# Kernel tuning notes

Measured on AMD Instinct MI355X. Metric: run time of the kernel, lower is better.

## Reference

```python
import jax, jax.numpy as jnp
import numpy as np

M0 = 0.5
M_MIN = 0.25
SCALE = 32.0
NUM_CLASSES = 100000
FEAT_DIM = 256
BATCH = 512


def setup_inputs() -> dict:
    key = jax.random.key(0)
    k1, k2, k3, k4 = jax.random.split(key, 4)
    features = jax.random.normal(k1, (BATCH, FEAT_DIM), dtype=jnp.float32)
    labels = jax.random.randint(k2, (BATCH,), 0, NUM_CLASSES, dtype=jnp.int64)
    weights = jax.random.uniform(k3, (BATCH,), dtype=jnp.float32)
    # xavier_uniform for (num_classes, feat_dim)
    limit = float(np.sqrt(6.0 / (NUM_CLASSES + FEAT_DIM)))
    weight = jax.random.uniform(k4, (NUM_CLASSES, FEAT_DIM), dtype=jnp.float32,
                                minval=-limit, maxval=limit)
    return {"features": features, "weight": weight, "weights": weights, "labels": labels}


def reference(features, weight, weights, labels):
    B = features.shape[0]
    norms = jnp.linalg.norm(features, axis=1)  # (B,)
    lo = jax.lax.stop_gradient(norms.min())
    hi = jax.lax.stop_gradient(norms.max())
    denom = jnp.maximum(hi - lo, 1e-8)
    margins = jnp.clip(M_MIN + (M0 - M_MIN) * (norms - lo) / denom, M_MIN, M0)  # (B,)

    feat_n = features / jnp.maximum(norms, 1e-12)[:, None]
    w_n = weight / jnp.maximum(jnp.linalg.norm(weight, axis=1), 1e-12)[:, None]
    cosine = jnp.clip(feat_n @ w_n.T, -1.0 + 1e-7, 1.0 - 1e-7)  # (B, C)

    rows = jnp.arange(B)
    cos_t = cosine[rows, labels]                      # target cosine (B,)
    theta_t = jnp.arccos(cos_t)
    cos_m_t = cos_t * jnp.cos(margins) - jnp.sin(theta_t) * jnp.sin(margins)

    logits = SCALE * cosine
    logits = logits.at[rows, labels].set(SCALE * cos_m_t)

    logp = jax.nn.log_softmax(logits, axis=1)
    per_sample = -logp[rows, labels]
    return (per_sample * weights).mean()
```

## Files before the change

kernel.cpp:

```cpp
#include <hip/hip_runtime.h>
#include <hip/hip_bf16.h>
#include <math.h>

#define BATCH 512
#define FEAT  256
#define NCLS  100000
#define SCALE_ 32.0f
#define M0_    0.5f
#define MMIN_  0.25f

#define BN 32
#define NT32 3125
#define NSLOTS 256
#define NPART 256
#define K4CHUNK 16
#define NK4 (NPART / K4CHUNK)

#define LOG2E_ 1.44269504088896f
#define K2C_   (SCALE_ * LOG2E_)

typedef unsigned short u16;
typedef short s16x8 __attribute__((ext_vector_type(8)));
typedef float f32x4 __attribute__((ext_vector_type(4)));

__device__ u16   g_fbf16[BATCH * FEAT];
__device__ float g_norms[BATCH];
__device__ float g_dot[BATCH];
__device__ float g_wn2[BATCH];
__device__ float g_psum[NPART * BATCH];
__device__ float g_qs[NK4 * BATCH];

__device__ __forceinline__ u16 f2b(float x) {
  union { float f; unsigned u; } v; v.f = x;
  unsigned r = v.u + 0x7FFFu + ((v.u >> 16) & 1u);
  return (u16)(r >> 16);
}

__device__ __forceinline__ unsigned pkbf16(float a, float b) {
  unsigned r;
  asm("v_cvt_pk_bf16_f32 %0, %1, %2" : "=v"(r) : "v"(a), "v"(b));
  return r;
}

__device__ __forceinline__ float ex2(float x) {
  return __builtin_amdgcn_exp2f(x);
}

__global__ void k12(const float* __restrict__ feat, const float* __restrict__ wmat,
                    const void* __restrict__ labels) {
  int b = blockIdx.x;
  int wid = threadIdx.x >> 6, lane = threadIdx.x & 63;
  if (b < 128) {
    int row = b * 4 + wid;
    float4 f = ((const float4*)(feat + row * FEAT))[lane];
    float ss = f.x * f.x + f.y * f.y + f.z * f.z + f.w * f.w;
    #pragma unroll
    for (int d = 1; d < 64; d <<= 1) ss += __shfl_xor(ss, d, 64);
    float nrm = sqrtf(ss);
    float inv = 1.0f / fmaxf(nrm, 1e-12f);
    ushort4 h;
    h.x = f2b(f.x * inv); h.y = f2b(f.y * inv);
    h.z = f2b(f.z * inv); h.w = f2b(f.w * inv);
    ((ushort4*)(g_fbf16 + row * FEAT))[lane] = h;
    if (lane == 0) g_norms[row] = nrm;
  } else {
    int i = (b - 128) * 4 + wid;
    const int* labw = (const int*)labels;
    int odd = 0;
    #pragma unroll
    for (int k = 0; k < 4; ++k) odd |= labw[2 * (k * 64 + lane) + 1];
    unsigned long long bl = __ballot(odd != 0);
    long long lab;
    if (bl != 0ULL) lab = (long long)((const int*)labels)[i];
    else            lab = ((const long long*)labels)[i];
    float4 a = ((const float4*)(feat + i * FEAT))[lane];
    float4 w = ((const float4*)(wmat + (size_t)lab * FEAT))[lane];
    float d  = a.x * w.x + a.y * w.y + a.z * w.z + a.w * w.w;
    float bb = w.x * w.x + w.y * w.y + w.z * w.z + w.w * w.w;
    #pragma unroll
    for (int t = 1; t < 64; t <<= 1) {
      d  += __shfl_xor(d, t, 64);
      bb += __shfl_xor(bb, t, 64);
    }
    if (lane == 0) { g_dot[i] = d; g_wn2[i] = bb; }
  }
}


#define LOADC(TILE) do {                                                    \
    rowL_ = tid >> 4;                                                       \
    const float4* s0_ = (const float4*)(wmat + (size_t)((TILE) * BN + rowL_) * FEAT + (tid & 15) * 16);      \
    const float4* s1_ = (const float4*)(wmat + (size_t)((TILE) * BN + 16 + rowL_) * FEAT + (tid & 15) * 16); \
    v_[0] = s0_[0]; v_[1] = s0_[1]; v_[2] = s0_[2]; v_[3] = s0_[3];         \
    v_[4] = s1_[0]; v_[5] = s1_[1]; v_[6] = s1_[2]; v_[7] = s1_[3];         \
  } while (0)

#define FINHALF(NB, G, ROW) do {                                            \
    float ss_ = 0.0f;                                                       \
    _Pragma("unroll")                                                       \
    for (int k_ = 0; k_ < 4; ++k_) {                                        \
      float4 vv_ = v_[(G) * 4 + k_];                                        \
      ss_ += vv_.x * vv_.x + vv_.y * vv_.y + vv_.z * vv_.z + vv_.w * vv_.w; \
    }                                                                       \
    ss_ += __shfl_xor(ss_, 1, 64);                                          \
    ss_ += __shfl_xor(ss_, 2, 64);                                          \
    ss_ += __shfl_xor(ss_, 4, 64);                                          \
    ss_ += __shfl_xor(ss_, 8, 64);                                          \
    float inv_ = 1.0f / fmaxf(sqrtf(ss_), 1e-12f);                          \
    u16* dst_ = &Ws[NB][0] + (ROW) * FEAT;                                  \
    _Pragma("unroll")                                                       \
    for (int k_ = 0; k_ < 2; ++k_) {                                        \
      int jj_ = (tid & 15) * 2 + k_;                                        \
      float4 va_ = v_[(G) * 4 + 2 * k_], vb_ = v_[(G) * 4 + 2 * k_ + 1];    \
      int4 w4_;                                                             \
      w4_.x = (int)pkbf16(va_.x * inv_, va_.y * inv_);                      \
      w4_.y = (int)pkbf16(va_.z * inv_, va_.w * inv_);                      \
      w4_.z = (int)pkbf16(vb_.x * inv_, vb_.y * inv_);                      \
      w4_.w = (int)pkbf16(vb_.z * inv_, vb_.w * inv_);                      \
      *(int4*)(dst_ + ((jj_ ^ ((ROW) & 7)) * 8)) = w4_;                     \
    }                                                                       \
  } while (0)

#define PHASE(p8) do {                                                      \
    f32x4 acc[4];                                                           \
    _Pragma("unroll")                                                       \
    for (int m = 0; m < 4; ++m) acc[m] = f32x4{0.0f, 0.0f, 0.0f, 0.0f};     \
    const u16* wb = &Ws[buf][0];                                            \
    const int row_ = (p8) * 16 + s;                                         \
    __builtin_amdgcn_s_setprio(1);                                          \
    _Pragma("unroll")                                                       \
    for (int c = 0; c < 8; ++c) {                                           \
      int cc = c * 4 + q;                                                   \
      s16x8 wf = *(const s16x8*)(wb + row_ * FEAT + (cc ^ (row_ & 7)) * 8); \
      _Pragma("unroll")                                                     \
      for (int m = 0; m < 4; ++m)                                           \
        acc[m] = __builtin_amdgcn_mfma_f32_16x16x32_bf16(wf, fr[m][c], acc[m], 0, 0, 0); \
    }                                                                       \
    __builtin_amdgcn_s_setprio(0);                                          \
    _Pragma("unroll")                                                       \
    for (int m = 0; m < 4; ++m) {                                           \
      float sl = ex2(fmaf(acc[m][0], K2C_, -K2C_))                          \
               + ex2(fmaf(acc[m][1], K2C_, -K2C_))                          \
               + ex2(fmaf(acc[m][2], K2C_, -K2C_))                          \
               + ex2(fmaf(acc[m][3], K2C_, -K2C_));                         \
      S[m] += sl;                                                           \
    }                                                                       \
  } while (0)

__global__ __launch_bounds__(256, 1) void k3(const float* __restrict__ wmat) {
  __shared__ __align__(16) u16 Ws[2][BN * FEAT];

  const int tid  = threadIdx.x;
  const int lane = tid & 63, wid = tid >> 6;
  const int s = lane & 15, q = lane >> 4;
  const int bid = blockIdx.x;
  const int nslot = bid & 255;
  const int sh = bid >> 8;
  const int niter = ((NT32 - 1 - nslot) >> 8) + 1;

  int rowL_;
  float4 v_[8];

  LOADC(nslot);
  FINHALF(0, 0, rowL_);
  FINHALF(0, 1, 16 + rowL_);

  s16x8 fr[4][8];
  {
    const int srow = sh * 256 + wid * 64;
    #pragma unroll
    for (int m = 0; m < 4; ++m)
      #pragma unroll
      for (int c = 0; c < 8; ++c)
        fr[m][c] = *(const s16x8*)(g_fbf16 + (srow + m * 16 + s) * FEAT + c * 32 + q * 8);
  }

  float S[4] = {0.0f, 0.0f, 0.0f, 0.0f};

  __syncthreads();

  int buf = 0;
  for (int t = 0; t < niter; ++t) {
    const bool last = (t + 1 == niter);

    if (!last) LOADC(nslot + (t + 1) * NSLOTS);
    PHASE(0);
    if (!last) FINHALF(buf ^ 1, 0, rowL_);
    PHASE(1);
    if (!last) FINHALF(buf ^ 1, 1, 16 + rowL_);
    __syncthreads();
    buf ^= 1;
  }

  #pragma unroll
  for (int m = 0; m < 4; ++m) {
    S[m] += __shfl_xor(S[m], 16, 64);
    S[m] += __shfl_xor(S[m], 32, 64);
  }

  if (lane < 16) {
    #pragma unroll
    for (int m = 0; m < 4; ++m) {
      int smp = sh * 256 + wid * 64 + m * 16 + lane;
      g_psum[nslot * BATCH + smp] = S[m];
    }
  }
}

__global__ __launch_bounds__(512) void k4a() {
  int i = threadIdx.x;
  int b = blockIdx.x;
  float S = 0.0f;
  #pragma unroll 4
  for (int p = b * K4CHUNK; p < b * K4CHUNK + K4CHUNK; ++p)
    S += g_psum[p * BATCH + i];
  g_qs[b * BATCH + i] = S;
}

__global__ void k4b(const float* __restrict__ wts, float* __restrict__ out) {
  int i = threadIdx.x;
  float S = 0.0f;
  #pragma unroll
  for (int t = 0; t < NK4; ++t) S += g_qs[t * BATCH + i];

  float n = g_norms[i];
  __shared__ float smin[512], smax[512];
  smin[i] = n; smax[i] = n;
  __syncthreads();
  for (int st = 256; st > 0; st >>= 1) {
    if (i < st) {
      smin[i] = fminf(smin[i], smin[i + st]);
      smax[i] = fmaxf(smax[i], smax[i + st]);
    }
    __syncthreads();
  }
  float lo = smin[0], hi = smax[0];
  float denom = fmaxf(hi - lo, 1e-8f);
  float mg = MMIN_ + (M0_ - MMIN_) * (n - lo) / denom;
  mg = fminf(fmaxf(mg, MMIN_), M0_);

  const float CLIP = 1.0f - 1e-7f;
  float wn = fmaxf(sqrtf(g_wn2[i]), 1e-12f);
  float ct = g_dot[i] / (fmaxf(n, 1e-12f) * wn);
  ct = fminf(fmaxf(ct, -CLIP), CLIP);

  float sint = sqrtf(fmaxf(0.0f, 1.0f - ct * ct));
  float cosm = ct * cosf(mg) - sint * sinf(mg);
  float b_old = K2C_ * ct;
  float b_new = K2C_ * cosm;
  float S2 = S - ex2(b_old - K2C_) + ex2(b_new - K2C_);
  float lse = 32.0f + logf(S2);
  float contrib = (lse - SCALE_ * cosm) * wts[i];
  __shared__ float sred[512];
  sred[i] = contrib;
  __syncthreads();
  for (int st = 256; st > 0; st >>= 1) {
    if (i < st) sred[i] += sred[i + st];
    __syncthreads();
  }
  if (i == 0) out[0] = sred[0] * (1.0f / (float)BATCH);
}

extern "C" void kernel_launch(void* const* d_in, const int* in_sizes, int n_in,
                              void* d_out, int out_size, void* d_ws, size_t ws_size,
                              hipStream_t stream) {
  const float* feat = (const float*)d_in[0];
  const float* wmat = (const float*)d_in[1];
  const float* wts  = (const float*)d_in[2];
  const void*  labs = d_in[3];
  float* out = (float*)d_out;

  hipLaunchKernelGGL(k12, dim3(256), dim3(256), 0, stream, feat, wmat, labs);
  hipLaunchKernelGGL(k3,  dim3(512), dim3(256), 0, stream, wmat);
  hipLaunchKernelGGL(k4a, dim3(NK4), dim3(512), 0, stream);
  hipLaunchKernelGGL(k4b, dim3(1), dim3(512), 0, stream, wts, out);
}
```

Measured before the change: 54.86 us.

## Double class tile to 64 rows with interleaved half-tile prefetch

Increases the class tile size from 32 to 64 rows, so each iteration runs four MFMA phases and interleaves two half-tile loads and normalizations between them. This halves the number of block barriers and loop iterations per class processed. Because 100000 is not a multiple of 64, it adds clamped row loads and masking of out-of-range columns on the last tile. Fewer, larger tiles risk more load imbalance across the 256 slots and double the shared-memory footprint.

```diff
diff --git a/kernel.cpp b/kernel.cpp
--- a/kernel.cpp
+++ b/kernel.cpp
@@ -9,8 +9,8 @@
 #define M0_    0.5f
 #define MMIN_  0.25f
 
-#define BN 32
-#define NT32 3125
+#define BN 64
+#define NT64 1563
 #define NSLOTS 256
 #define NPART 256
 #define K4CHUNK 16
@@ -87,10 +87,14 @@
 }
 
 
-#define LOADC(TILE) do {                                                    \
+#define LOADC(TILE, RB) do {                                                \
     rowL_ = tid >> 4;                                                       \
-    const float4* s0_ = (const float4*)(wmat + (size_t)((TILE) * BN + rowL_) * FEAT + (tid & 15) * 16);      \
-    const float4* s1_ = (const float4*)(wmat + (size_t)((TILE) * BN + 16 + rowL_) * FEAT + (tid & 15) * 16); \
+    int r0_ = (TILE) * BN + (RB) + rowL_;                                   \
+    int r1_ = r0_ + 16;                                                     \
+    r0_ = r0_ < NCLS ? r0_ : NCLS - 1;                                      \
+    r1_ = r1_ < NCLS ? r1_ : NCLS - 1;                                      \
+    const float4* s0_ = (const float4*)(wmat + (size_t)r0_ * FEAT + (tid & 15) * 16); \
+    const float4* s1_ = (const float4*)(wmat + (size_t)r1_ * FEAT + (tid & 15) * 16); \
     v_[0] = s0_[0]; v_[1] = s0_[1]; v_[2] = s0_[2]; v_[3] = s0_[3];         \
     v_[4] = s1_[0]; v_[5] = s1_[1]; v_[6] = s1_[2]; v_[7] = s1_[3];         \
   } while (0)
@@ -121,6 +125,11 @@
     }                                                                       \
   } while (0)
 
+#define FINISHC(NB, RB) do {                                                \
+    FINHALF(NB, 0, (RB) + rowL_);                                           \
+    FINHALF(NB, 1, (RB) + 16 + rowL_);                                      \
+  } while (0)
+
 #define PHASE(p8) do {                                                      \
     f32x4 acc[4];                                                           \
     _Pragma("unroll")                                                       \
@@ -139,11 +148,18 @@
     __builtin_amdgcn_s_setprio(0);                                          \
     _Pragma("unroll")                                                       \
     for (int m = 0; m < 4; ++m) {                                           \
-      float sl = ex2(fmaf(acc[m][0], K2C_, -K2C_))                          \
-               + ex2(fmaf(acc[m][1], K2C_, -K2C_))                          \
-               + ex2(fmaf(acc[m][2], K2C_, -K2C_))                          \
-               + ex2(fmaf(acc[m][3], K2C_, -K2C_));                         \
-      S[m] += sl;                                                           \
+      float t0_ = ex2(fmaf(acc[m][0], K2C_, -K2C_));                        \
+      float t1_ = ex2(fmaf(acc[m][1], K2C_, -K2C_));                        \
+      float t2_ = ex2(fmaf(acc[m][2], K2C_, -K2C_));                        \
+      float t3_ = ex2(fmaf(acc[m][3], K2C_, -K2C_));                        \
+      if (edge) {                                                           \
+        int cb_ = tile * BN + (p8) * 16 + q * 4;                            \
+        if (cb_ + 0 >= NCLS) t0_ = 0.0f;                                    \
+        if (cb_ + 1 >= NCLS) t1_ = 0.0f;                                    \
+        if (cb_ + 2 >= NCLS) t2_ = 0.0f;                                    \
+        if (cb_ + 3 >= NCLS) t3_ = 0.0f;                                    \
+      }                                                                     \
+      S[m] += (t0_ + t1_) + (t2_ + t3_);                                    \
     }                                                                       \
   } while (0)
 
@@ -156,14 +172,13 @@
   const int bid = blockIdx.x;
   const int nslot = bid & 255;
   const int sh = bid >> 8;
-  const int niter = ((NT32 - 1 - nslot) >> 8) + 1;
+  const int niter = ((NT64 - 1 - nslot) >> 8) + 1;
 
   int rowL_;
   float4 v_[8];
 
-  LOADC(nslot);
-  FINHALF(0, 0, rowL_);
-  FINHALF(0, 1, 16 + rowL_);
+  LOADC(nslot, 0);  FINISHC(0, 0);
+  LOADC(nslot, 32); FINISHC(0, 32);
 
   s16x8 fr[4][8];
   {
@@ -182,12 +197,17 @@
   int buf = 0;
   for (int t = 0; t < niter; ++t) {
     const bool last = (t + 1 == niter);
-
-    if (!last) LOADC(nslot + (t + 1) * NSLOTS);
+    const int tile = nslot + t * NSLOTS;
+    const bool edge = (tile == NT64 - 1);
+    const int ntile = nslot + (t + 1) * NSLOTS;
+
+    if (!last) LOADC(ntile, 0);
     PHASE(0);
-    if (!last) FINHALF(buf ^ 1, 0, rowL_);
+    if (!last) { FINISHC(buf ^ 1, 0); LOADC(ntile, 32); }
     PHASE(1);
-    if (!last) FINHALF(buf ^ 1, 1, 16 + rowL_);
+    PHASE(2);
+    if (!last) FINISHC(buf ^ 1, 32);
+    PHASE(3);
     __syncthreads();
     buf ^= 1;
   }
```

Measured after the change: 67.73 us. 1.23x slower.
